# Performance work log

Hardware: AMD Instinct MI355X
Metric: run time of the kernel (lower is better)

Reference implementation:

```python
import jax, jax.numpy as jnp
import numpy as np

CLASS_NUM, EMBED_DIM, N = 16, 64, 256


def setup_inputs() -> dict:
    key = jax.random.key(0)
    ks = jax.random.split(key, 5)
    return {
        "query": jax.random.normal(ks[0], (CLASS_NUM, EMBED_DIM, N), dtype=jnp.float32),
        "key": jax.random.normal(ks[1], (CLASS_NUM, EMBED_DIM, N), dtype=jnp.float32),
        "value": jax.random.normal(ks[2], (CLASS_NUM, EMBED_DIM, N), dtype=jnp.float32),
        "W_out": jax.random.normal(ks[3], (EMBED_DIM, EMBED_DIM), dtype=jnp.float32) * 0.02,
        "b_out": jax.random.normal(ks[4], (EMBED_DIM,), dtype=jnp.float32) * 0.02,
    }


def reference(query, key, value, W_out, b_out):
    C, E, N_ = query.shape
    scale = 1.0 / jnp.sqrt(jnp.float32(E))
    # head_dim==1 attention: scores are an outer product over the token axis
    # scores[c,e,i,j] = q[c,e,i] * k[c,e,j] / sqrt(E)   -> (C, E, N, N)
    scores = query[..., :, None] * key[..., None, :] * scale
    attn = jax.nn.softmax(scores, axis=-1)
    # out[c,e,i] = sum_j attn[c,e,i,j] * v[c,e,j]
    out = jnp.einsum("cenm,cem->cen", attn, value)
    # torch: reshape (C,E,N,1) -> (-1, E) row-major, then Linear
    out = out.reshape(-1, E)
    return out @ W_out.T + b_out
```

## Files before the change

### kernel.cpp

```cpp
#include <hip/hip_runtime.h>
#include <math.h>

#define C_NUM 16
#define E_DIM 64
#define N_TOK 256

#define K_SCALE (0.125f * 1.4426950408889634f)

#if __has_builtin(__builtin_amdgcn_exp2f)
#define EXP2(x) __builtin_amdgcn_exp2f(x)
#else
#define EXP2(x) exp2f(x)
#endif

__global__ __launch_bounds__(256) void xattn_fused_kernel(
    const float* __restrict__ q, const float* __restrict__ k,
    const float* __restrict__ v, const float* __restrict__ W,
    const float* __restrict__ bias, float* __restrict__ out)
{
    __shared__ __align__(16) float o[N_TOK];
    __shared__ float Wl[E_DIM * 66];

    const int blk  = blockIdx.x;
    const int tid  = threadIdx.x;
    const int base = blk * N_TOK;

    float wreg[16];
    #pragma unroll
    for (int r = 0; r < 16; ++r)
        wreg[r] = W[tid + r * 256];

    const float qs = q[base + tid] * K_SCALE;

    float se0 = 0.f, se1 = 0.f, se2 = 0.f, se3 = 0.f;
    float sv0 = 0.f, sv1 = 0.f, sv2 = 0.f, sv3 = 0.f;
    const float4* kb4 = reinterpret_cast<const float4*>(k + base);
    const float4* vb4 = reinterpret_cast<const float4*>(v + base);
    #pragma unroll 4
    for (int j4 = 0; j4 < N_TOK / 4; ++j4) {
        const float4 kv4 = kb4[j4];
        const float4 vv4 = vb4[j4];
        const float e0 = EXP2(qs * kv4.x);
        const float e1 = EXP2(qs * kv4.y);
        const float e2 = EXP2(qs * kv4.z);
        const float e3 = EXP2(qs * kv4.w);
        se0 += e0; sv0 = fmaf(e0, vv4.x, sv0);
        se1 += e1; sv1 = fmaf(e1, vv4.y, sv1);
        se2 += e2; sv2 = fmaf(e2, vv4.z, sv2);
        se3 += e3; sv3 = fmaf(e3, vv4.w, sv3);
    }
    o[tid] = ((sv0 + sv1) + (sv2 + sv3)) / ((se0 + se1) + (se2 + se3));

    #pragma unroll
    for (int r = 0; r < 16; ++r) {
        const int idx = tid + r * 256;
        Wl[(idx >> 6) * 66 + (idx & 63)] = wreg[r];
    }
    __syncthreads();

    const int d  = tid & 63;
    const int rl = tid >> 6;
    const float2* orow = reinterpret_cast<const float2*>(&o[rl * 64]);
    const float2* wrow = reinterpret_cast<const float2*>(&Wl[d * 66]);
    float acc0 = bias[d], acc1 = 0.f;
    #pragma unroll
    for (int kk = 0; kk < 32; ++kk) {
        const float2 ov = orow[kk];
        const float2 wv = wrow[kk];
        acc0 = fmaf(ov.x, wv.x, acc0);
        acc1 = fmaf(ov.y, wv.y, acc1);
    }
    out[base + tid] = acc0 + acc1;
}

extern "C" void kernel_launch(void* const* d_in, const int* in_sizes, int n_in,
                              void* d_out, int out_size, void* d_ws, size_t ws_size,
                              hipStream_t stream) {
    const float* q    = (const float*)d_in[0];
    const float* k    = (const float*)d_in[1];
    const float* v    = (const float*)d_in[2];
    const float* W    = (const float*)d_in[3];
    const float* bias = (const float*)d_in[4];
    float* out = (float*)d_out;

    xattn_fused_kernel<<<dim3(C_NUM * E_DIM), dim3(256), 0, stream>>>(
        q, k, v, W, bias, out);
}
```

Baseline: 74.93 us.

## Split key axis across two thread halves with shared-memory reduction

Doubles the block to 512 threads. Each half processes half of the key/value tokens and writes partial exp-sums and weighted sums to shared memory, which are combined before normalisation. The output projection is likewise split over the reduction dimension and summed through shared memory. This adds parallelism and halves the serial exp loop per thread, at the cost of extra shared memory, two more barriers, and more LDS traffic.

```diff
diff --git a/kernel.cpp b/kernel.cpp
--- a/kernel.cpp
+++ b/kernel.cpp
@@ -13,31 +13,35 @@
 #define EXP2(x) exp2f(x)
 #endif
 
-__global__ __launch_bounds__(256) void xattn_fused_kernel(
+__global__ __launch_bounds__(512, 8) void xattn_fused_kernel(
     const float* __restrict__ q, const float* __restrict__ k,
     const float* __restrict__ v, const float* __restrict__ W,
     const float* __restrict__ bias, float* __restrict__ out)
 {
-    __shared__ __align__(16) float o[N_TOK];
+    __shared__ __align__(16) float2 psum[512];
+    __shared__ __align__(16) float  o[N_TOK];
+    __shared__ float eacc[512];
     __shared__ float Wl[E_DIM * 66];
 
     const int blk  = blockIdx.x;
     const int tid  = threadIdx.x;
+    const int i    = tid & 255;
+    const int h    = tid >> 8;
     const int base = blk * N_TOK;
 
-    float wreg[16];
+    float wreg[8];
     #pragma unroll
-    for (int r = 0; r < 16; ++r)
-        wreg[r] = W[tid + r * 256];
+    for (int r = 0; r < 8; ++r)
+        wreg[r] = W[tid + r * 512];
 
-    const float qs = q[base + tid] * K_SCALE;
+    const float qs = q[base + i] * K_SCALE;
 
     float se0 = 0.f, se1 = 0.f, se2 = 0.f, se3 = 0.f;
     float sv0 = 0.f, sv1 = 0.f, sv2 = 0.f, sv3 = 0.f;
-    const float4* kb4 = reinterpret_cast<const float4*>(k + base);
-    const float4* vb4 = reinterpret_cast<const float4*>(v + base);
+    const float4* kb4 = reinterpret_cast<const float4*>(k + base + h * 128);
+    const float4* vb4 = reinterpret_cast<const float4*>(v + base + h * 128);
     #pragma unroll 4
-    for (int j4 = 0; j4 < N_TOK / 4; ++j4) {
+    for (int j4 = 0; j4 < 32; ++j4) {
         const float4 kv4 = kb4[j4];
         const float4 vv4 = vb4[j4];
         const float e0 = EXP2(qs * kv4.x);
@@ -49,28 +53,41 @@
         se2 += e2; sv2 = fmaf(e2, vv4.z, sv2);
         se3 += e3; sv3 = fmaf(e3, vv4.w, sv3);
     }
-    o[tid] = ((sv0 + sv1) + (sv2 + sv3)) / ((se0 + se1) + (se2 + se3));
+    psum[tid] = make_float2((se0 + se1) + (se2 + se3),
+                            (sv0 + sv1) + (sv2 + sv3));
 
     #pragma unroll
-    for (int r = 0; r < 16; ++r) {
-        const int idx = tid + r * 256;
+    for (int r = 0; r < 8; ++r) {
+        const int idx = tid + r * 512;
         Wl[(idx >> 6) * 66 + (idx & 63)] = wreg[r];
     }
     __syncthreads();
 
+    if (tid < 256) {
+        const float2 a = psum[tid];
+        const float2 b = psum[tid + 256];
+        o[tid] = (a.y + b.y) / (a.x + b.x);
+    }
+    __syncthreads();
+
     const int d  = tid & 63;
-    const int rl = tid >> 6;
-    const float2* orow = reinterpret_cast<const float2*>(&o[rl * 64]);
-    const float2* wrow = reinterpret_cast<const float2*>(&Wl[d * 66]);
-    float acc0 = bias[d], acc1 = 0.f;
+    const int rl = (tid >> 6) & 3;
+    const float2* orow = reinterpret_cast<const float2*>(&o[rl * 64]) + h * 16;
+    const float2* wrow = reinterpret_cast<const float2*>(&Wl[d * 66]) + h * 16;
+    float acc0 = h ? 0.f : bias[d];
+    float acc1 = 0.f;
     #pragma unroll
-    for (int kk = 0; kk < 32; ++kk) {
+    for (int kk = 0; kk < 16; ++kk) {
         const float2 ov = orow[kk];
         const float2 wv = wrow[kk];
         acc0 = fmaf(ov.x, wv.x, acc0);
         acc1 = fmaf(ov.y, wv.y, acc1);
     }
-    out[base + tid] = acc0 + acc1;
+    eacc[tid] = acc0 + acc1;
+    __syncthreads();
+
+    if (tid < 256)
+        out[base + tid] = eacc[tid] + eacc[tid + 256];
 }
 
 extern "C" void kernel_launch(void* const* d_in, const int* in_sizes, int n_in,
@@ -83,6 +100,6 @@
     const float* bias = (const float*)d_in[4];
     float* out = (float*)d_out;
 
-    xattn_fused_kernel<<<dim3(C_NUM * E_DIM), dim3(256), 0, stream>>>(
+    xattn_fused_kernel<<<dim3(C_NUM * E_DIM), dim3(512), 0, stream>>>(
         q, k, v, W, bias, out);
 }
```

New measurement: 78.09 us. 4.2% more time.

## Split each row across four blocks and partition key axis across warps

Applied to the files above, without the earlier changes.

Each (c,e) row is now handled by four blocks, each covering 64 query tokens. Within a block the four wavefronts each process a quarter of the key axis, and partial softmax sums are combined through shared memory. The output projection is likewise split along the reduction dimension across waves and reduced in LDS. This shortens each thread's serial exp loop and launches four times as many blocks, at the cost of loading W four times as often per row plus extra barriers and LDS traffic.

```diff
diff --git a/kernel.cpp b/kernel.cpp
--- a/kernel.cpp
+++ b/kernel.cpp
@@ -13,31 +13,32 @@
 #define EXP2(x) exp2f(x)
 #endif
 
-__global__ __launch_bounds__(256) void xattn_fused_kernel(
+__global__ __launch_bounds__(256, 8) void xattn_fused_kernel(
     const float* __restrict__ q, const float* __restrict__ k,
     const float* __restrict__ v, const float* __restrict__ W,
     const float* __restrict__ bias, float* __restrict__ out)
 {
-    __shared__ __align__(16) float o[N_TOK];
+    __shared__ __align__(16) float2 psum[4][64];
+    __shared__ __align__(16) float  o[64];
+    __shared__ float eacc[4][64];
     __shared__ float Wl[E_DIM * 66];
 
-    const int blk  = blockIdx.x;
+    const int bid  = blockIdx.x;
+    const int blk  = bid >> 2;
+    const int qd   = bid & 3;
     const int tid  = threadIdx.x;
+    const int il   = tid & 63;
+    const int h    = tid >> 6;
     const int base = blk * N_TOK;
 
-    float wreg[16];
-    #pragma unroll
-    for (int r = 0; r < 16; ++r)
-        wreg[r] = W[tid + r * 256];
-
-    const float qs = q[base + tid] * K_SCALE;
+    const float qs = q[base + qd * 64 + il] * K_SCALE;
 
     float se0 = 0.f, se1 = 0.f, se2 = 0.f, se3 = 0.f;
     float sv0 = 0.f, sv1 = 0.f, sv2 = 0.f, sv3 = 0.f;
-    const float4* kb4 = reinterpret_cast<const float4*>(k + base);
-    const float4* vb4 = reinterpret_cast<const float4*>(v + base);
+    const float4* kb4 = reinterpret_cast<const float4*>(k + base + h * 64);
+    const float4* vb4 = reinterpret_cast<const float4*>(v + base + h * 64);
     #pragma unroll 4
-    for (int j4 = 0; j4 < N_TOK / 4; ++j4) {
+    for (int j4 = 0; j4 < 16; ++j4) {
         const float4 kv4 = kb4[j4];
         const float4 vv4 = vb4[j4];
         const float e0 = EXP2(qs * kv4.x);
@@ -49,28 +50,42 @@
         se2 += e2; sv2 = fmaf(e2, vv4.z, sv2);
         se3 += e3; sv3 = fmaf(e3, vv4.w, sv3);
     }
-    o[tid] = ((sv0 + sv1) + (sv2 + sv3)) / ((se0 + se1) + (se2 + se3));
+    psum[h][il] = make_float2((se0 + se1) + (se2 + se3),
+                              (sv0 + sv1) + (sv2 + sv3));
+
+    __builtin_amdgcn_sched_barrier(0);
 
     #pragma unroll
     for (int r = 0; r < 16; ++r) {
         const int idx = tid + r * 256;
-        Wl[(idx >> 6) * 66 + (idx & 63)] = wreg[r];
+        Wl[(idx >> 6) * 66 + (idx & 63)] = W[idx];
     }
     __syncthreads();
 
-    const int d  = tid & 63;
-    const int rl = tid >> 6;
-    const float2* orow = reinterpret_cast<const float2*>(&o[rl * 64]);
-    const float2* wrow = reinterpret_cast<const float2*>(&Wl[d * 66]);
-    float acc0 = bias[d], acc1 = 0.f;
+    if (tid < 64) {
+        const float2 a = psum[0][tid], b = psum[1][tid];
+        const float2 c = psum[2][tid], d = psum[3][tid];
+        o[tid] = ((a.y + b.y) + (c.y + d.y)) / ((a.x + b.x) + (c.x + d.x));
+    }
+    __syncthreads();
+
+    const float2* orow = reinterpret_cast<const float2*>(o) + h * 8;
+    const float2* wrow = reinterpret_cast<const float2*>(&Wl[il * 66]) + h * 8;
+    float acc0 = h ? 0.f : bias[il];
+    float acc1 = 0.f;
     #pragma unroll
-    for (int kk = 0; kk < 32; ++kk) {
+    for (int kk = 0; kk < 8; ++kk) {
         const float2 ov = orow[kk];
         const float2 wv = wrow[kk];
         acc0 = fmaf(ov.x, wv.x, acc0);
         acc1 = fmaf(ov.y, wv.y, acc1);
     }
-    out[base + tid] = acc0 + acc1;
+    eacc[h][il] = acc0 + acc1;
+    __syncthreads();
+
+    if (tid < 64)
+        out[base + qd * 64 + tid] = (eacc[0][tid] + eacc[1][tid])
+                                  + (eacc[2][tid] + eacc[3][tid]);
 }
 
 extern "C" void kernel_launch(void* const* d_in, const int* in_sizes, int n_in,
@@ -83,6 +98,6 @@
     const float* bias = (const float*)d_in[4];
     float* out = (float*)d_out;
 
-    xattn_fused_kernel<<<dim3(C_NUM * E_DIM), dim3(256), 0, stream>>>(
+    xattn_fused_kernel<<<dim3(C_NUM * E_DIM * 4), dim3(256), 0, stream>>>(
         q, k, v, W, bias, out);
 }
```

Measured after the change: 79.16 us. 1.06x slower.
